# Kernel tuning notes

Measured on AMD Instinct MI355X. Metric: run time of the kernel, lower is better.

The kernel has to match this reference:

```python
import jax, jax.numpy as jnp
import numpy as np
import math

P = 2
TAU = 1.0
USE_POW = False
ALIGN_W = 1.0
ENTROPY_W = 1.0
EPS = 1e-12


def _pairwise_l2(z):
    # torch.cdist(z, z, p=2): sqrt of squared distances via GEMM decomposition
    sq = jnp.sum(z * z, axis=-1)  # [N]
    d2 = sq[:, None] + sq[None, :] - 2.0 * (z @ z.T)  # [N, N]
    d = jnp.sqrt(jnp.maximum(d2, 0.0))
    return jnp.maximum(d, EPS)  # clamp_min(eps)


def setup_inputs() -> dict:
    key = jax.random.key(0)
    k0, k1 = jax.random.split(key)
    v0 = jax.random.normal(k0, (8192, 256), dtype=jnp.float32)
    v1 = jax.random.normal(k1, (8192, 256), dtype=jnp.float32)
    return {"v0": v0, "v1": v1}


def reference(v0, v1):
    views = [v0, v1]
    n = v0.shape[0]

    # Alignment term: mean Lp distance between matched rows, one pair (0,1)
    diff = v0 - v1
    align = jnp.sqrt(jnp.sum(diff * diff, axis=-1)).mean()  # p=2 norm per row

    # Entropy term: masked logsumexp over within-view pairwise distances
    log_num_neg = math.log(n - 1)
    eye = jnp.eye(n, dtype=bool)
    entropy = jnp.float32(0.0)
    for z in views:
        dist = _pairwise_l2(z)  # [N, N]
        logits = jnp.where(eye, -jnp.inf, -dist / TAU)
        lme = jax.nn.logsumexp(logits, axis=1) - log_num_neg  # [N]
        entropy = entropy + lme.mean()
    entropy = entropy / len(views)

    return ALIGN_W * align + ENTROPY_W * entropy
```

## Files before the change

kernel.cpp:

```cpp
#include <hip/hip_runtime.h>
#include <math.h>


#define D_DIM 256
#define NB 64
#define NSEG 1056
#define S_Q 26.0f
#define LOG2E2 2.0813689810f
#define LP 65

typedef int i32x4 __attribute__((ext_vector_type(4)));
typedef unsigned int u32;
#define AS1 __attribute__((address_space(1)))
#define AS3 __attribute__((address_space(3)))

__device__ inline void load_lds16(const void* g, void* l) {
  __builtin_amdgcn_global_load_lds((const AS1 u32*)g, (AS3 u32*)l, 16, 0, 0);
}

__device__ inline int q8(float x) {
  return __float2int_rn(fminf(fmaxf(x * S_Q, -127.0f), 127.0f));
}
__device__ inline u32 q8x4(const float4 f) {
  return (u32)(q8(f.x) & 255) | ((u32)(q8(f.y) & 255) << 8) |
         ((u32)(q8(f.z) & 255) << 16) | ((u32)(q8(f.w) & 255) << 24);
}

__device__ inline int Gfun(int M) {
  const int m = M >> 1;
  return (M & 1) ? (m + 1) * (m + 1) : m * (m + 1);
}

__global__ __launch_bounds__(256) void prep(
    const float* __restrict__ v0, const float* __restrict__ v1,
    unsigned char* __restrict__ ph0, unsigned char* __restrict__ ph1,
    float* __restrict__ sq0, float* __restrict__ sq1,
    float* __restrict__ S0, float* __restrict__ S1,
    float* __restrict__ align_part) {
  __shared__ float4 l0[16 * LP], l1[16 * LP];
  __shared__ float red0[4][16], red1[4][16], red2[4][16];
  const int R = blockIdx.x;
  const int t = threadIdx.x;

  #pragma unroll
  for (int p = 0; p < 4; ++p) {
    const int slot = t + p * 256;
    const int r = slot >> 6, col = slot & 63;
    const size_t g = (size_t)(R * 16 + r) * 64 + col;
    l0[r * LP + col] = ((const float4*)v0)[g];
    l1[r * LP + col] = ((const float4*)v1)[g];
  }
  __syncthreads();

  {
    const int rr = t & 15, c = t >> 4;
    const int s = c >> 2, q = c & 3;
    const int li = rr * LP + c * 4;
    uint4 u0, u1;
    u0.x = q8x4(l0[li + 0]); u0.y = q8x4(l0[li + 1]);
    u0.z = q8x4(l0[li + 2]); u0.w = q8x4(l0[li + 3]);
    u1.x = q8x4(l1[li + 0]); u1.y = q8x4(l1[li + 1]);
    u1.z = q8x4(l1[li + 2]); u1.w = q8x4(l1[li + 3]);
    const size_t dst = (size_t)(R * 4 + s) * 64 + q * 16 + rr;
    ((uint4*)ph0)[dst] = u0;
    ((uint4*)ph1)[dst] = u1;
  }

  {
    const int rr = t & 15;
    const int base = rr * LP + (t >> 4) * 4;
    float s0p = 0.f, s1p = 0.f, s2p = 0.f;
    #pragma unroll
    for (int c = 0; c < 4; ++c) {
      const float4 a = l0[base + c], b = l1[base + c];
      s0p += a.x * a.x + a.y * a.y + a.z * a.z + a.w * a.w;
      s1p += b.x * b.x + b.y * b.y + b.z * b.z + b.w * b.w;
      const float dx = a.x - b.x, dy = a.y - b.y, dz = a.z - b.z, dw = a.w - b.w;
      s2p += dx * dx + dy * dy + dz * dz + dw * dw;
    }
    s0p += __shfl_xor(s0p, 16, 64); s0p += __shfl_xor(s0p, 32, 64);
    s1p += __shfl_xor(s1p, 16, 64); s1p += __shfl_xor(s1p, 32, 64);
    s2p += __shfl_xor(s2p, 16, 64); s2p += __shfl_xor(s2p, 32, 64);
    const int w = t >> 6, lane = t & 63;
    if (lane < 16) { red0[w][lane] = s0p; red1[w][lane] = s1p; red2[w][lane] = s2p; }
  }
  __syncthreads();
  if (t < 16) {
    const int row = R * 16 + t;
    const float a0 = red0[0][t] + red0[1][t] + red0[2][t] + red0[3][t];
    const float a1 = red1[0][t] + red1[1][t] + red1[2][t] + red1[3][t];
    const float a2 = red2[0][t] + red2[1][t] + red2[2][t] + red2[3][t];
    sq0[row] = a0 * LOG2E2;
    sq1[row] = a1 * LOG2E2;
    align_part[row] = sqrtf(a2);
    S0[row] = 0.0f;
    S1[row] = 0.0f;
  }
}

__global__ __launch_bounds__(256) void entropy_tile(
    const unsigned char* __restrict__ ph0, const unsigned char* __restrict__ ph1,
    const float* __restrict__ sq0, const float* __restrict__ sq1,
    float* __restrict__ S0, float* __restrict__ S1) {
  const unsigned char* __restrict__ ph = blockIdx.y ? ph1 : ph0;
  const float* __restrict__ sq = blockIdx.y ? sq1 : sq0;
  float* __restrict__ S        = blockIdx.y ? S1 : S0;

  const int lin = blockIdx.x;
  int bi = 0;
  while (NSEG - Gfun(64 - (bi + 1)) <= lin) ++bi;
  const int q = lin - (NSEG - Gfun(64 - bi));
  const int bj0 = bi + 2 * q;

  __shared__ __align__(16) char smem[32768];
  float* swp = (float*)smem;

  const int t = threadIdx.x, lane = t & 63, w = t >> 6;
  const int wi = w >> 1, wj = w & 1;
  const int quad = lane >> 4, l15 = lane & 15;
  const int i0 = bi * 128;

  #pragma unroll
  for (int r8 = 0; r8 < 8; ++r8) {
    const int seg = w * 8 + r8;
    const unsigned char* src = ph + (size_t)bi * 32768 + seg * 1024 + lane * 16;
    load_lds16(src, smem + seg * 1024);
  }
  __syncthreads();

  const i32x4* __restrict__ phv = (const i32x4*)ph;
  const i32x4* smemv = (const i32x4*)smem;
  const float K2 = 2.0f * LOG2E2 / (S_Q * S_Q);

  float prow[4][4];
  #pragma unroll
  for (int m = 0; m < 4; ++m)
    #pragma unroll
    for (int r = 0; r < 4; ++r) prow[m][r] = 0.f;

  auto do_tile = [&](const int bj, const bool diag_t) {
    const int j0 = bj * 128;
    const int baseB = ((bj * 8 + wj * 4) * 4) * 64 + lane;

    float sjl[4];
    #pragma unroll
    for (int n = 0; n < 4; ++n) sjl[n] = sq[j0 + wj * 64 + n * 16 + l15];

    i32x4 bF[2][4];
    #pragma unroll
    for (int n = 0; n < 4; ++n) bF[0][n] = phv[baseB + (n * 4) * 64];

    i32x4 acc[4][4];
    #pragma unroll
    for (int m = 0; m < 4; ++m)
      #pragma unroll
      for (int n = 0; n < 4; ++n) acc[m][n] = (i32x4){0, 0, 0, 0};

    #pragma unroll
    for (int s = 0; s < 4; ++s) {
      const int cur = s & 1, nxt = cur ^ 1;
      if (s < 3) {
        #pragma unroll
        for (int n = 0; n < 4; ++n)
          bF[nxt][n] = phv[baseB + (n * 4 + s + 1) * 64];
      }
      i32x4 ah[4];
      #pragma unroll
      for (int m = 0; m < 4; ++m)
        ah[m] = smemv[(size_t)((wi * 4 + m) * 4 + s) * 64 + lane];
      #pragma unroll
      for (int m = 0; m < 4; ++m)
        #pragma unroll
        for (int n = 0; n < 4; ++n)
          acc[m][n] = __builtin_amdgcn_mfma_i32_16x16x64_i8(ah[m], bF[cur][n], acc[m][n], 0, 0, 0);
    }

    float csum[4] = {0.f, 0.f, 0.f, 0.f};
    #pragma unroll
    for (int m = 0; m < 4; ++m) {
      #pragma unroll
      for (int r = 0; r < 4; ++r) {
        const int rowl = m * 16 + quad * 4 + r;
        const int gi = i0 + wi * 64 + rowl;
        const float si = sq[gi];
        float p = 0.f;
        #pragma unroll
        for (int n = 0; n < 4; ++n) {
          const float d2 = fmaf(-K2, (float)acc[m][n][r], si + sjl[n]);
          float e = __builtin_amdgcn_exp2f(-__builtin_amdgcn_sqrtf(d2));
          if (diag_t && gi == j0 + wj * 64 + n * 16 + l15) e = 0.f;
          p += e;
          csum[n] += e;
        }
        prow[m][r] += p;
      }
    }
    if (!diag_t) {
      #pragma unroll
      for (int n = 0; n < 4; ++n) {
        float c2 = csum[n];
        c2 += __shfl_xor(c2, 16, 64);
        c2 += __shfl_xor(c2, 32, 64);
        if (quad == 0) atomicAdd(&S[j0 + wj * 64 + n * 16 + l15], c2);
      }
    }
  };

  if (bj0 == bi) do_tile(bi, true); else do_tile(bj0, false);
  if (bj0 + 1 < NB) do_tile(bj0 + 1, false);

  __syncthreads();

  const int wbase = w * 1088;
  #pragma unroll
  for (int m = 0; m < 4; ++m)
    #pragma unroll
    for (int r = 0; r < 4; ++r)
      swp[wbase + (m * 16 + quad * 4 + r) * 17 + l15] = prow[m][r];
  float rs = 0.f;
  #pragma unroll
  for (int j = 0; j < 16; ++j) rs += swp[wbase + lane * 17 + j];
  atomicAdd(&S[i0 + wi * 64 + lane], rs);
}

__global__ __launch_bounds__(256) void finalize_part(
    const float* __restrict__ S0, const float* __restrict__ S1,
    const float* __restrict__ align_part,
    float* __restrict__ part_log, float* __restrict__ part_align) {
  __shared__ float shl[4], sha[4];
  const int t = threadIdx.x, lane = t & 63, w = t >> 6;
  const int idx = blockIdx.x * 256 + t;
  float lg = __logf(S0[idx]) + __logf(S1[idx]);
  float al = align_part[idx];
  #pragma unroll
  for (int o = 1; o < 64; o <<= 1) {
    lg += __shfl_xor(lg, o, 64);
    al += __shfl_xor(al, o, 64);
  }
  if (lane == 0) { shl[w] = lg; sha[w] = al; }
  __syncthreads();
  if (t == 0) {
    part_log[blockIdx.x] = shl[0] + shl[1] + shl[2] + shl[3];
    part_align[blockIdx.x] = sha[0] + sha[1] + sha[2] + sha[3];
  }
}

__global__ void finalize_final(const float* __restrict__ part_log,
                               const float* __restrict__ part_align,
                               float* __restrict__ out, int n) {
  const int lane = threadIdx.x & 63;
  double lg = (lane < 32) ? (double)part_log[lane] : 0.0;
  double al = (lane < 32) ? (double)part_align[lane] : 0.0;
  #pragma unroll
  for (int o = 1; o < 32; o <<= 1) {
    lg += __shfl_xor(lg, o, 64);
    al += __shfl_xor(al, o, 64);
  }
  if (lane == 0) {
    double align = al / (double)n;
    double entropy = 0.5 * lg / (double)n - log((double)(n - 1));
    out[0] = (float)(align + entropy);
  }
}

extern "C" void kernel_launch(void* const* d_in, const int* in_sizes, int n_in,
                              void* d_out, int out_size, void* d_ws, size_t ws_size,
                              hipStream_t stream) {
  const float* v0 = (const float*)d_in[0];
  const float* v1 = (const float*)d_in[1];
  float* out = (float*)d_out;
  const int n = in_sizes[0] / D_DIM;

  float* ws         = (float*)d_ws;
  float* sq0        = ws;
  float* sq1        = ws + n;
  float* S0         = ws + 2 * n;
  float* S1         = ws + 3 * n;
  float* align_part = ws + 4 * n;
  float* part_log   = ws + 5 * n;
  float* part_align = ws + 5 * n + 32;
  unsigned char* ph0 = (unsigned char*)(ws + 5 * n + 64);
  unsigned char* ph1 = ph0 + (size_t)n * D_DIM;

  prep<<<n / 16, 256, 0, stream>>>(v0, v1, ph0, ph1, sq0, sq1, S0, S1, align_part);

  dim3 grid(NSEG, 2);
  entropy_tile<<<grid, 256, 0, stream>>>(ph0, ph1, sq0, sq1, S0, S1);

  finalize_part<<<n / 256, 256, 0, stream>>>(S0, S1, align_part, part_log, part_align);
  finalize_final<<<1, 64, 0, stream>>>(part_log, part_align, out, n);
}
```

Baseline: 112.8 us.

## Interleave per-m-block MFMA compute with exp/sqrt epilogue using ping-pong accumulators

Restructures the tile loop so the B fragments for all four k-steps are preloaded and the 4x4 MFMA accumulation is split into per-row-block (m) chunks. Two accumulator sets alternate so the transcendental epilogue of one block can overlap the MFMAs of the next. This cuts accumulator register pressure from 16 to 8 vectors and overlaps matrix-core and VALU work. In exchange, all B fragments are held in registers at once, and the A fragment is now loaded separately for each m-block.

```diff
diff --git a/kernel.cpp b/kernel.cpp
--- a/kernel.cpp
+++ b/kernel.cpp
@@ -146,47 +146,41 @@
     #pragma unroll
     for (int n = 0; n < 4; ++n) sjl[n] = sq[j0 + wj * 64 + n * 16 + l15];
 
-    i32x4 bF[2][4];
-    #pragma unroll
-    for (int n = 0; n < 4; ++n) bF[0][n] = phv[baseB + (n * 4) * 64];
-
-    i32x4 acc[4][4];
-    #pragma unroll
-    for (int m = 0; m < 4; ++m)
-      #pragma unroll
-      for (int n = 0; n < 4; ++n) acc[m][n] = (i32x4){0, 0, 0, 0};
-
-    #pragma unroll
-    for (int s = 0; s < 4; ++s) {
-      const int cur = s & 1, nxt = cur ^ 1;
-      if (s < 3) {
+    i32x4 bF[4][4];
+    #pragma unroll
+    for (int s = 0; s < 4; ++s)
+      #pragma unroll
+      for (int n = 0; n < 4; ++n)
+        bF[s][n] = phv[baseB + (n * 4 + s) * 64];
+
+    float csum[4] = {0.f, 0.f, 0.f, 0.f};
+
+    i32x4 accA[4], accB[4];
+    float siA[4], siB[4];
+
+    auto compute = [&](i32x4* acc, float* si, const int m) {
+      #pragma unroll
+      for (int r = 0; r < 4; ++r)
+        si[r] = sq[i0 + wi * 64 + m * 16 + quad * 4 + r];
+      #pragma unroll
+      for (int n = 0; n < 4; ++n) acc[n] = (i32x4){0, 0, 0, 0};
+      #pragma unroll
+      for (int s = 0; s < 4; ++s) {
+        const i32x4 ah = smemv[(size_t)((wi * 4 + m) * 4 + s) * 64 + lane];
         #pragma unroll
         for (int n = 0; n < 4; ++n)
-          bF[nxt][n] = phv[baseB + (n * 4 + s + 1) * 64];
+          acc[n] = __builtin_amdgcn_mfma_i32_16x16x64_i8(ah, bF[s][n], acc[n], 0, 0, 0);
       }
-      i32x4 ah[4];
-      #pragma unroll
-      for (int m = 0; m < 4; ++m)
-        ah[m] = smemv[(size_t)((wi * 4 + m) * 4 + s) * 64 + lane];
-      #pragma unroll
-      for (int m = 0; m < 4; ++m)
-        #pragma unroll
-        for (int n = 0; n < 4; ++n)
-          acc[m][n] = __builtin_amdgcn_mfma_i32_16x16x64_i8(ah[m], bF[cur][n], acc[m][n], 0, 0, 0);
-    }
-
-    float csum[4] = {0.f, 0.f, 0.f, 0.f};
-    #pragma unroll
-    for (int m = 0; m < 4; ++m) {
+    };
+
+    auto epilogue = [&](const i32x4* acc, const float* si, const int m) {
       #pragma unroll
       for (int r = 0; r < 4; ++r) {
-        const int rowl = m * 16 + quad * 4 + r;
-        const int gi = i0 + wi * 64 + rowl;
-        const float si = sq[gi];
+        const int gi = i0 + wi * 64 + m * 16 + quad * 4 + r;
         float p = 0.f;
         #pragma unroll
         for (int n = 0; n < 4; ++n) {
-          const float d2 = fmaf(-K2, (float)acc[m][n][r], si + sjl[n]);
+          const float d2 = fmaf(-K2, (float)acc[n][r], si[r] + sjl[n]);
           float e = __builtin_amdgcn_exp2f(-__builtin_amdgcn_sqrtf(d2));
           if (diag_t && gi == j0 + wj * 64 + n * 16 + l15) e = 0.f;
           p += e;
@@ -194,7 +188,17 @@
         }
         prow[m][r] += p;
       }
-    }
+    };
+
+    compute(accA, siA, 0);
+    compute(accB, siB, 1);
+    epilogue(accA, siA, 0);
+    compute(accA, siA, 2);
+    epilogue(accB, siB, 1);
+    compute(accB, siB, 3);
+    epilogue(accA, siA, 2);
+    epilogue(accB, siB, 3);
+
     if (!diag_t) {
       #pragma unroll
       for (int n = 0; n < 4; ++n) {
```

New measurement: 112.7 us. Within noise of the previous version (-0.0%).
